# Performance work log

Hardware: AMD Instinct MI355X
Metric: run time of the kernel (lower is better)

## Reference

```python
import jax, jax.numpy as jnp
import numpy as np

N = 50000      # nodes
E = 800000     # edges per relation/layer
L = 2          # GCN layer_num
D = 128        # input_dim == output_dim


def setup_inputs() -> dict:
    key = jax.random.key(0)
    ks = jax.random.split(key, 11)
    x = jax.random.normal(ks[0], (N, D), jnp.float32)
    hidden = jax.random.normal(ks[1], (N, D), jnp.float32)
    adj_src = jax.random.randint(ks[2], (L, E), 0, N)
    adj_dst = jax.random.randint(ks[3], (L, E), 0, N)
    adj_w = jax.random.uniform(ks[4], (L, E), jnp.float32)
    std = 1.0 / np.sqrt(D)  # reset_parameters: uniform(-std, std)
    def u(k, shape):
        return jax.random.uniform(k, shape, jnp.float32, -std, std)
    gcn_W = u(ks[5], (L, D, D))
    gcn_b = u(ks[6], (L, D))
    x2h_W = u(ks[7], (D, 3 * D))
    x2h_b = u(ks[8], (3 * D,))
    h2h_W = u(ks[9], (D, 3 * D))
    h2h_b = u(ks[10], (3 * D,))
    return dict(x=x, hidden=hidden, adj_src=adj_src, adj_dst=adj_dst, adj_w=adj_w,
                gcn_W=gcn_W, gcn_b=gcn_b, x2h_W=x2h_W, x2h_b=x2h_b,
                h2h_W=h2h_W, h2h_b=h2h_b)


def reference(x, hidden, adj_src, adj_dst, adj_w, gcn_W, gcn_b,
              x2h_W, x2h_b, h2h_W, h2h_b):
    # MRGCN: layer_num GCN layers, layer l uses relation l's sparse adjacency.
    h = x
    for l in range(L):
        support = h @ gcn_W[l]                              # [N, D]
        msg = support[adj_src[l]] * adj_w[l][:, None]       # [E, D] irregular gather
        agg = jax.ops.segment_sum(msg, adj_dst[l], num_segments=N)  # spmm scatter-add
        h = jax.nn.relu(agg + gcn_b[l])
    # GRU gate chain (dropout=0 / eval mode)
    gate_x = h @ x2h_W + x2h_b                              # [N, 3D]
    gate_h = hidden @ h2h_W + h2h_b                         # [N, 3D]
    i_r, i_i, i_n = jnp.split(gate_x, 3, axis=1)
    h_r, h_i, h_n = jnp.split(gate_h, 3, axis=1)
    resetgate = jax.nn.sigmoid(i_r + h_r)
    inputgate = jax.nn.sigmoid(i_i + h_i)
    newgate = jnp.tanh(i_n + resetgate * h_n)
    hy = newgate + inputgate * (hidden - newgate)
    return hy
```

## Files before the change

### kernel.cpp

```cpp
#include <hip/hip_runtime.h>

#define D 128
#define RPW 8
#define ROWS_PB 32

typedef __attribute__((ext_vector_type(8))) short short8;
typedef __attribute__((ext_vector_type(4))) float f32x4;

static __device__ __forceinline__ ushort f2bf(float f) {
    unsigned u = __float_as_uint(f);
    unsigned r = (u + 0x7fffu + ((u >> 16) & 1u)) >> 16;
    return (ushort)r;
}

__global__ __launch_bounds__(256) void gemm_rowbatch(const float* __restrict__ in,
                                                     const float* __restrict__ W,
                                                     float* __restrict__ out, int N) {
    __shared__ float sw[D * D];
    __shared__ float sh[ROWS_PB][D];
    int tid = threadIdx.x;
    int row0 = blockIdx.x * ROWS_PB;
    for (int j = tid; j < D * D / 4; j += 256)
        ((float4*)sw)[j] = ((const float4*)W)[j];
    for (int i = tid; i < ROWS_PB * (D / 4); i += 256) {
        int r = i >> 5, c4 = i & 31;
        int row = row0 + r;
        float4 v = (row < N) ? ((const float4*)(in + (size_t)row * D))[c4]
                             : make_float4(0.f, 0.f, 0.f, 0.f);
        ((float4*)sh)[i] = v;
    }
    __syncthreads();
    int wid = tid >> 6, lane = tid & 63;
    int rb = wid * RPW;
    float acc0[RPW], acc1[RPW];
#pragma unroll
    for (int r = 0; r < RPW; ++r) { acc0[r] = 0.f; acc1[r] = 0.f; }
    for (int k = 0; k < D; k += 4) {
        float w0[4], w1[4];
#pragma unroll
        for (int kk = 0; kk < 4; ++kk) {
            w0[kk] = sw[(k + kk) * D + lane];
            w1[kk] = sw[(k + kk) * D + lane + 64];
        }
#pragma unroll
        for (int r = 0; r < RPW; ++r) {
            float4 a4 = *(const float4*)&sh[rb + r][k];
            acc0[r] = fmaf(a4.x, w0[0], acc0[r]); acc1[r] = fmaf(a4.x, w1[0], acc1[r]);
            acc0[r] = fmaf(a4.y, w0[1], acc0[r]); acc1[r] = fmaf(a4.y, w1[1], acc1[r]);
            acc0[r] = fmaf(a4.z, w0[2], acc0[r]); acc1[r] = fmaf(a4.z, w1[2], acc1[r]);
            acc0[r] = fmaf(a4.w, w0[3], acc0[r]); acc1[r] = fmaf(a4.w, w1[3], acc1[r]);
        }
    }
#pragma unroll
    for (int r = 0; r < RPW; ++r) {
        int row = row0 + rb + r;
        if (row < N) {
            out[(size_t)row * D + lane] = acc0[r];
            out[(size_t)row * D + lane + 64] = acc1[r];
        }
    }
}

__global__ void zero_int4(int4* __restrict__ p, int n4) {
    int i = blockIdx.x * blockDim.x + threadIdx.x;
    if (i < n4) p[i] = make_int4(0, 0, 0, 0);
}

__global__ void slot_kernel(const int* __restrict__ dst, int* __restrict__ counts,
                            ushort* __restrict__ pl, int E2, int E, int N) {
    int i = blockIdx.x * blockDim.x + threadIdx.x;
    if (i >= E2) return;
    int off = (i >= E) ? N : 0;
    pl[i] = (ushort)atomicAdd(&counts[off + dst[i]], 1);
}

__global__ __launch_bounds__(256) void scan_partial(const int4* __restrict__ counts4,
                                                    int* __restrict__ bsum) {
    int b = blockIdx.x, t = threadIdx.x;
    int4 c0 = counts4[(size_t)b * 512 + t * 2];
    int4 c1 = counts4[(size_t)b * 512 + t * 2 + 1];
    int s = c0.x + c0.y + c0.z + c0.w + c1.x + c1.y + c1.z + c1.w;
#pragma unroll
    for (int d = 1; d < 64; d <<= 1) s += __shfl_xor(s, d);
    __shared__ int ws[4];
    if ((t & 63) == 0) ws[t >> 6] = s;
    __syncthreads();
    if (t == 0) bsum[b] = ws[0] + ws[1] + ws[2] + ws[3];
}

__global__ void scan_base(const int* __restrict__ bsum, int* __restrict__ bbase, int nb) {
    int lane = threadIdx.x;
    int run = 0;
    for (int c = 0; c < nb; c += 64) {
        int v = (c + lane < nb) ? bsum[c + lane] : 0;
        int inc = v;
#pragma unroll
        for (int d = 1; d < 64; d <<= 1) {
            int y = __shfl_up(inc, d);
            if (lane >= d) inc += y;
        }
        if (c + lane < nb) bbase[c + lane] = run + inc - v;
        run += __shfl(inc, 63);
    }
}

__global__ __launch_bounds__(256) void scan_apply(const int4* __restrict__ counts4,
                                                  const int* __restrict__ bbase,
                                                  int4* __restrict__ off4) {
    __shared__ int ts[256];
    int b = blockIdx.x, t = threadIdx.x;
    int4 c0 = counts4[(size_t)b * 512 + t * 2];
    int4 c1 = counts4[(size_t)b * 512 + t * 2 + 1];
    int s = c0.x + c0.y + c0.z + c0.w + c1.x + c1.y + c1.z + c1.w;
    ts[t] = s;
    __syncthreads();
    for (int d = 1; d < 256; d <<= 1) {
        int x = ts[t];
        int y = (t >= d) ? ts[t - d] : 0;
        __syncthreads();
        ts[t] = x + y;
        __syncthreads();
    }
    int base = bbase[b] + ((t == 0) ? 0 : ts[t - 1]);
    int4 o0, o1;
    o0.x = base;
    o0.y = o0.x + c0.x;
    o0.z = o0.y + c0.y;
    o0.w = o0.z + c0.z;
    o1.x = o0.w + c0.w;
    o1.y = o1.x + c1.x;
    o1.z = o1.y + c1.y;
    o1.w = o1.z + c1.z;
    off4[(size_t)b * 512 + t * 2] = o0;
    off4[(size_t)b * 512 + t * 2 + 1] = o1;
}

__global__ void place_kernel(const int* __restrict__ src, const int* __restrict__ dst,
                             const float* __restrict__ w, const int* __restrict__ offsets,
                             const ushort* __restrict__ pl, int sub,
                             int2* __restrict__ srcw, int E) {
    int e = blockIdx.x * blockDim.x + threadIdx.x;
    if (e >= E) return;
    int p = offsets[dst[e]] - sub + (int)pl[e];
    srcw[p] = make_int2(src[e], __float_as_int(w[e]));
}

__global__ void gather_nodes(const float* __restrict__ sup, const int2* __restrict__ srcw,
                             const int* __restrict__ offsets, int sub,
                             const float* __restrict__ bias,
                             float* __restrict__ out, int N) {
    int node = (blockIdx.x * blockDim.x + threadIdx.x) >> 6;
    int lane = threadIdx.x & 63;
    if (node >= N) return;
    int lo = offsets[node] - sub, hi = offsets[node + 1] - sub;
    float ax = 0.f, ay = 0.f;
    int c = lane * 2;
    int j = lo;
    for (; j + 8 <= hi; j += 8) {
        int2 s[8];
        float2 v[8];
#pragma unroll
        for (int u = 0; u < 8; ++u) s[u] = srcw[j + u];
#pragma unroll
        for (int u = 0; u < 8; ++u)
            v[u] = *(const float2*)(sup + (size_t)s[u].x * D + c);
#pragma unroll
        for (int u = 0; u < 8; ++u) {
            float wt = __int_as_float(s[u].y);
            ax = fmaf(wt, v[u].x, ax);
            ay = fmaf(wt, v[u].y, ay);
        }
    }
    for (; j < hi; ++j) {
        int2 sw = srcw[j];
        float wt = __int_as_float(sw.y);
        float2 v = *(const float2*)(sup + (size_t)sw.x * D + c);
        ax = fmaf(wt, v.x, ax); ay = fmaf(wt, v.y, ay);
    }
    float2 bi = *(const float2*)(bias + c);
    float2 o;
    o.x = fmaxf(ax + bi.x, 0.f);
    o.y = fmaxf(ay + bi.y, 0.f);
    *(float2*)(out + (size_t)node * D + c) = o;
}

__global__ void convW(const float* __restrict__ Wx, const float* __restrict__ Wh,
                      ushort* __restrict__ wxt, ushort* __restrict__ wht) {
    int i = blockIdx.x * blockDim.x + threadIdx.x;
    if (i >= 384 * 128) return;
    int c = i >> 7, k = i & 127;
    wxt[i] = f2bf(Wx[(size_t)k * 384 + c]);
    wht[i] = f2bf(Wh[(size_t)k * 384 + c]);
}

#define QROWS 192
#define KPAD 136
__global__ __launch_bounds__(256) void gru_mfma_lds(const float* __restrict__ h,
                                                    const float* __restrict__ hidden,
                                                    const ushort* __restrict__ wxt,
                                                    const ushort* __restrict__ wht,
                                                    const float* __restrict__ bx,
                                                    const float* __restrict__ bh,
                                                    float* __restrict__ out, int N) {
    __shared__ ushort lw[QROWS * KPAD];
    int tid = threadIdx.x;
    int wid = tid >> 6, lane = tid & 63;
    int nstripes = (N + 15) >> 4;
    int stripe = blockIdx.x * 4 + wid;
    bool live = stripe < nstripes;
    int row0 = stripe * 16;
    int lr = lane & 15;
    int lk = (lane >> 4) * 8;

    short8 Ah[4], Ad[4];
    if (live) {
        const float* hrow = h + (size_t)(row0 + lr) * D + lk;
        const float* drow = hidden + (size_t)(row0 + lr) * D + lk;
#pragma unroll
        for (int ks = 0; ks < 4; ++ks) {
            float4 a0 = *(const float4*)(hrow + ks * 32);
            float4 a1 = *(const float4*)(hrow + ks * 32 + 4);
            float4 c0 = *(const float4*)(drow + ks * 32);
            float4 c1 = *(const float4*)(drow + ks * 32 + 4);
            short8 va, vc;
            va[0] = f2bf(a0.x); va[1] = f2bf(a0.y); va[2] = f2bf(a0.z); va[3] = f2bf(a0.w);
            va[4] = f2bf(a1.x); va[5] = f2bf(a1.y); va[6] = f2bf(a1.z); va[7] = f2bf(a1.w);
            vc[0] = f2bf(c0.x); vc[1] = f2bf(c0.y); vc[2] = f2bf(c0.z); vc[3] = f2bf(c0.w);
            vc[4] = f2bf(c1.x); vc[5] = f2bf(c1.y); vc[6] = f2bf(c1.z); vc[7] = f2bf(c1.w);
            Ah[ks] = va;
            Ad[ks] = vc;
        }
    }
    int orow = row0 + (lane >> 4) * 4;

    for (int q = 0; q < 4; ++q) {
        if (q) __syncthreads();
        for (int j = tid; j < QROWS * 16; j += 256) {
            int chunk = j & 15;
            int row = j >> 4;
            int mat = row >= 96;
            int r = row - (mat ? 96 : 0);
            int g = r >> 5;
            int c = r & 31;
            const ushort* srcp = (mat ? wht : wxt)
                               + ((size_t)(g * 128 + q * 32 + c) << 7) + (chunk << 3);
            *(short8*)&lw[row * KPAD + chunk * 8] = *(const short8*)srcp;
        }
        __syncthreads();
        if (!live) continue;

#pragma unroll
        for (int mt = 0; mt < 2; ++mt) {
            int cl = mt * 16 + lr;
            const ushort* bx0 = lw + (0 * 32 + cl) * KPAD + lk;
            const ushort* bx1 = lw + (1 * 32 + cl) * KPAD + lk;
            const ushort* bx2 = lw + (2 * 32 + cl) * KPAD + lk;
            const ushort* bh0 = lw + ((96 + 0 * 32) + cl) * KPAD + lk;
            const ushort* bh1 = lw + ((96 + 1 * 32) + cl) * KPAD + lk;
            const ushort* bh2 = lw + ((96 + 2 * 32) + cl) * KPAD + lk;
            f32x4 ax0{}, ax1{}, ax2{}, ah0{}, ah1{}, ah2{};
#pragma unroll
            for (int ks = 0; ks < 4; ++ks) {
                short8 w0 = *(const short8*)(bx0 + ks * 32);
                short8 w1 = *(const short8*)(bx1 + ks * 32);
                short8 w2 = *(const short8*)(bx2 + ks * 32);
                short8 v0 = *(const short8*)(bh0 + ks * 32);
                short8 v1 = *(const short8*)(bh1 + ks * 32);
                short8 v2 = *(const short8*)(bh2 + ks * 32);
                ax0 = __builtin_amdgcn_mfma_f32_16x16x32_bf16(Ah[ks], w0, ax0, 0, 0, 0);
                ax1 = __builtin_amdgcn_mfma_f32_16x16x32_bf16(Ah[ks], w1, ax1, 0, 0, 0);
                ax2 = __builtin_amdgcn_mfma_f32_16x16x32_bf16(Ah[ks], w2, ax2, 0, 0, 0);
                ah0 = __builtin_amdgcn_mfma_f32_16x16x32_bf16(Ad[ks], v0, ah0, 0, 0, 0);
                ah1 = __builtin_amdgcn_mfma_f32_16x16x32_bf16(Ad[ks], v1, ah1, 0, 0, 0);
                ah2 = __builtin_amdgcn_mfma_f32_16x16x32_bf16(Ad[ks], v2, ah2, 0, 0, 0);
            }
            int col = q * 32 + mt * 16 + lr;
            float bxr = bx[col], bxi = bx[col + 128], bxn = bx[col + 256];
            float bhr = bh[col], bhi = bh[col + 128], bhn = bh[col + 256];
#pragma unroll
            for (int r = 0; r < 4; ++r) {
                int row = orow + r;
                if (row < N) {
                    float ir = ax0[r] + bxr, hr = ah0[r] + bhr;
                    float ii = ax1[r] + bxi, hi = ah1[r] + bhi;
                    float in_ = ax2[r] + bxn, hn = ah2[r] + bhn;
                    float rg = 1.f / (1.f + __expf(-(ir + hr)));
                    float ig = 1.f / (1.f + __expf(-(ii + hi)));
                    float nx = in_ + rg * hn;
                    float ng = 1.f - 2.f / (__expf(2.f * nx) + 1.f);
                    float hv = hidden[(size_t)row * D + col];
                    out[(size_t)row * D + col] = ng + ig * (hv - ng);
                }
            }
        }
    }
}

extern "C" void kernel_launch(void* const* d_in, const int* in_sizes, int n_in,
                              void* d_out, int out_size, void* d_ws, size_t ws_size,
                              hipStream_t stream) {
    const float* x      = (const float*)d_in[0];
    const float* hidden = (const float*)d_in[1];
    const int*   adj_src = (const int*)d_in[2];
    const int*   adj_dst = (const int*)d_in[3];
    const float* adj_w   = (const float*)d_in[4];
    const float* gcn_W   = (const float*)d_in[5];
    const float* gcn_b   = (const float*)d_in[6];
    const float* x2h_W   = (const float*)d_in[7];
    const float* x2h_b   = (const float*)d_in[8];
    const float* h2h_W   = (const float*)d_in[9];
    const float* h2h_b   = (const float*)d_in[10];
    float* out = (float*)d_out;

    const int L = 2;
    const int N = in_sizes[0] / D;
    const int E = in_sizes[2] / L;
    const size_t nd = (size_t)N * D;

    const int twoN   = 2 * N;
    const int NB     = (twoN + 2047) / 2048;
    const int padded = NB * 2048;

    char* ws = (char*)d_ws;
    float* A        = (float*)ws;                 ws += nd * 4;
    float* B        = (float*)ws;                 ws += nd * 4;
    int*   counts2  = (int*)ws;                   ws += (size_t)padded * 4;
    int*   offsets2 = (int*)ws;                   ws += ((size_t)padded + 64) * 4;
    int*   bsum     = (int*)ws;                   ws += ((size_t)NB + 64) * 4;
    int*   bbase    = (int*)ws;                   ws += ((size_t)NB + 64) * 4;
    int2*  srcw     = (int2*)ws;                  ws += (size_t)E * 8;
    ushort* pl      = (ushort*)ws;                ws += (size_t)2 * E * 2;
    ushort* wxt     = (ushort*)ws;                ws += (size_t)384 * 128 * 2;
    ushort* wht     = (ushort*)ws;                ws += (size_t)384 * 128 * 2;

    dim3 blk(256);
    int batch_blocks = (N + ROWS_PB - 1) / ROWS_PB;
    int gat_blocks   = (N + 3) / 4;
    int edge_blocks  = (E + 255) / 256;
    int e2_blocks    = (2 * E + 255) / 256;
    int zero_blocks  = (padded / 4 + 255) / 256;
    int convw_blocks = (384 * 128 + 255) / 256;
    int nstripes     = (N + 15) / 16;
    int gru_blocks   = (nstripes + 3) / 4;

    convW<<<convw_blocks, blk, 0, stream>>>(x2h_W, h2h_W, wxt, wht);

    zero_int4<<<zero_blocks, blk, 0, stream>>>((int4*)counts2, padded / 4);
    slot_kernel<<<e2_blocks, blk, 0, stream>>>(adj_dst, counts2, pl, 2 * E, E, N);
    scan_partial<<<NB, blk, 0, stream>>>((const int4*)counts2, bsum);
    scan_base<<<1, 64, 0, stream>>>(bsum, bbase, NB);
    scan_apply<<<NB, blk, 0, stream>>>((const int4*)counts2, bbase, (int4*)offsets2);

    const float* hcur = x;
    for (int l = 0; l < L; ++l) {
        gemm_rowbatch<<<batch_blocks, blk, 0, stream>>>(hcur, gcn_W + (size_t)l * D * D, A, N);
        place_kernel<<<edge_blocks, blk, 0, stream>>>(adj_src + (size_t)l * E,
                                                      adj_dst + (size_t)l * E,
                                                      adj_w + (size_t)l * E,
                                                      offsets2 + (size_t)l * N,
                                                      pl + (size_t)l * E, l * E,
                                                      srcw, E);
        gather_nodes<<<gat_blocks, blk, 0, stream>>>(A, srcw, offsets2 + (size_t)l * N, l * E,
                                                     gcn_b + (size_t)l * D, B, N);
        hcur = B;
    }
    gru_mfma_lds<<<gru_blocks, blk, 0, stream>>>(B, hidden, wxt, wht, x2h_b, h2h_b, out, N);
}
```

Baseline: 379.8 us.

## Store GCN support in bf16 and fuse setup kernels into one launch

The GCN support matrix is now written in bf16, which halves the bytes the irregular gather reads per edge. The first-layer GEMM, the slot-counting atomics and the GRU weight conversion are merged into one heterogeneous launch so they run concurrently. Edge placement for both layers is done in one kernel into separate buffers, which removes per-layer launches. The bf16 support reduces precision of the aggregated messages, and the fused kernel's large LDS allocation applies to the light atomic and convert blocks too, which may limit their occupancy.

Result: faster. 327.3 us (-13.8%).

```diff
diff --git a/kernel.cpp b/kernel.cpp
--- a/kernel.cpp
+++ b/kernel.cpp
@@ -13,13 +13,12 @@
     return (ushort)r;
 }
 
-__global__ __launch_bounds__(256) void gemm_rowbatch(const float* __restrict__ in,
-                                                     const float* __restrict__ W,
-                                                     float* __restrict__ out, int N) {
-    __shared__ float sw[D * D];
-    __shared__ float sh[ROWS_PB][D];
-    int tid = threadIdx.x;
-    int row0 = blockIdx.x * ROWS_PB;
+static __device__ __forceinline__ void gemm_body(float* sw, float (*sh)[D],
+                                                 const float* __restrict__ in,
+                                                 const float* __restrict__ W,
+                                                 ushort* __restrict__ outb,
+                                                 int N, int bid, int tid) {
+    int row0 = bid * ROWS_PB;
     for (int j = tid; j < D * D / 4; j += 256)
         ((float4*)sw)[j] = ((const float4*)W)[j];
     for (int i = tid; i < ROWS_PB * (D / 4); i += 256) {
@@ -55,23 +54,55 @@
     for (int r = 0; r < RPW; ++r) {
         int row = row0 + rb + r;
         if (row < N) {
-            out[(size_t)row * D + lane] = acc0[r];
-            out[(size_t)row * D + lane + 64] = acc1[r];
-        }
-    }
+            outb[(size_t)row * D + lane] = f2bf(acc0[r]);
+            outb[(size_t)row * D + lane + 64] = f2bf(acc1[r]);
+        }
+    }
+}
+
+__global__ __launch_bounds__(256) void fused_sgc(const float* __restrict__ x,
+                                                 const float* __restrict__ W0,
+                                                 ushort* __restrict__ Abf, int N,
+                                                 const int* __restrict__ adj_dst,
+                                                 int* __restrict__ counts,
+                                                 ushort* __restrict__ pl, int E2, int E,
+                                                 const float* __restrict__ Wx,
+                                                 const float* __restrict__ Wh,
+                                                 ushort* __restrict__ wxt,
+                                                 ushort* __restrict__ wht,
+                                                 int GB, int SB) {
+    __shared__ float sw[D * D];
+    __shared__ float sh[ROWS_PB][D];
+    int bid = blockIdx.x, tid = threadIdx.x;
+    if (bid < GB) {
+        gemm_body(sw, sh, x, W0, Abf, N, bid, tid);
+    } else if (bid < GB + SB) {
+        int i = (bid - GB) * 256 + tid;
+        if (i < E2) {
+            int off = (i >= E) ? N : 0;
+            pl[i] = (ushort)atomicAdd(&counts[off + adj_dst[i]], 1);
+        }
+    } else {
+        int i = (bid - GB - SB) * 256 + tid;
+        if (i < 384 * 128) {
+            int c = i >> 7, k = i & 127;
+            wxt[i] = f2bf(Wx[(size_t)k * 384 + c]);
+            wht[i] = f2bf(Wh[(size_t)k * 384 + c]);
+        }
+    }
+}
+
+__global__ __launch_bounds__(256) void gemm_rowbatch_bf(const float* __restrict__ in,
+                                                        const float* __restrict__ W,
+                                                        ushort* __restrict__ outb, int N) {
+    __shared__ float sw[D * D];
+    __shared__ float sh[ROWS_PB][D];
+    gemm_body(sw, sh, in, W, outb, N, blockIdx.x, threadIdx.x);
 }
 
 __global__ void zero_int4(int4* __restrict__ p, int n4) {
     int i = blockIdx.x * blockDim.x + threadIdx.x;
     if (i < n4) p[i] = make_int4(0, 0, 0, 0);
-}
-
-__global__ void slot_kernel(const int* __restrict__ dst, int* __restrict__ counts,
-                            ushort* __restrict__ pl, int E2, int E, int N) {
-    int i = blockIdx.x * blockDim.x + threadIdx.x;
-    if (i >= E2) return;
-    int off = (i >= E) ? N : 0;
-    pl[i] = (ushort)atomicAdd(&counts[off + dst[i]], 1);
 }
 
 __global__ __launch_bounds__(256) void scan_partial(const int4* __restrict__ counts4,
@@ -135,17 +166,22 @@
     off4[(size_t)b * 512 + t * 2 + 1] = o1;
 }
 
-__global__ void place_kernel(const int* __restrict__ src, const int* __restrict__ dst,
-                             const float* __restrict__ w, const int* __restrict__ offsets,
-                             const ushort* __restrict__ pl, int sub,
-                             int2* __restrict__ srcw, int E) {
-    int e = blockIdx.x * blockDim.x + threadIdx.x;
-    if (e >= E) return;
-    int p = offsets[dst[e]] - sub + (int)pl[e];
-    srcw[p] = make_int2(src[e], __float_as_int(w[e]));
-}
-
-__global__ void gather_nodes(const float* __restrict__ sup, const int2* __restrict__ srcw,
+__global__ void place2_kernel(const int* __restrict__ src, const int* __restrict__ dst,
+                              const float* __restrict__ w,
+                              const int* __restrict__ offsets2,
+                              const ushort* __restrict__ pl,
+                              int2* __restrict__ srcw0, int2* __restrict__ srcw1,
+                              int E, int E2, int N) {
+    int i = blockIdx.x * blockDim.x + threadIdx.x;
+    if (i >= E2) return;
+    int l1 = i >= E;
+    int node = dst[i];
+    int p = offsets2[(l1 ? N : 0) + node] - (l1 ? E : 0) + (int)pl[i];
+    int2 v = make_int2(src[i], __float_as_int(w[i]));
+    (l1 ? srcw1 : srcw0)[p] = v;
+}
+
+__global__ void gather_nodes(const ushort* __restrict__ supb, const int2* __restrict__ srcw,
                              const int* __restrict__ offsets, int sub,
                              const float* __restrict__ bias,
                              float* __restrict__ out, int N) {
@@ -155,42 +191,35 @@
     int lo = offsets[node] - sub, hi = offsets[node + 1] - sub;
     float ax = 0.f, ay = 0.f;
     int c = lane * 2;
+    const ushort* base = supb + c;
     int j = lo;
     for (; j + 8 <= hi; j += 8) {
         int2 s[8];
-        float2 v[8];
+        uint v[8];
 #pragma unroll
         for (int u = 0; u < 8; ++u) s[u] = srcw[j + u];
 #pragma unroll
         for (int u = 0; u < 8; ++u)
-            v[u] = *(const float2*)(sup + (size_t)s[u].x * D + c);
+            v[u] = *(const uint*)(base + ((size_t)s[u].x << 7));
 #pragma unroll
         for (int u = 0; u < 8; ++u) {
             float wt = __int_as_float(s[u].y);
-            ax = fmaf(wt, v[u].x, ax);
-            ay = fmaf(wt, v[u].y, ay);
+            ax = fmaf(wt, __uint_as_float(v[u] << 16), ax);
+            ay = fmaf(wt, __uint_as_float(v[u] & 0xffff0000u), ay);
         }
     }
     for (; j < hi; ++j) {
         int2 sw = srcw[j];
         float wt = __int_as_float(sw.y);
-        float2 v = *(const float2*)(sup + (size_t)sw.x * D + c);
-        ax = fmaf(wt, v.x, ax); ay = fmaf(wt, v.y, ay);
+        uint v = *(const uint*)(base + ((size_t)sw.x << 7));
+        ax = fmaf(wt, __uint_as_float(v << 16), ax);
+        ay = fmaf(wt, __uint_as_float(v & 0xffff0000u), ay);
     }
     float2 bi = *(const float2*)(bias + c);
     float2 o;
     o.x = fmaxf(ax + bi.x, 0.f);
     o.y = fmaxf(ay + bi.y, 0.f);
     *(float2*)(out + (size_t)node * D + c) = o;
-}
-
-__global__ void convW(const float* __restrict__ Wx, const float* __restrict__ Wh,
-                      ushort* __restrict__ wxt, ushort* __restrict__ wht) {
-    int i = blockIdx.x * blockDim.x + threadIdx.x;
-    if (i >= 384 * 128) return;
-    int c = i >> 7, k = i & 127;
-    wxt[i] = f2bf(Wx[(size_t)k * 384 + c]);
-    wht[i] = f2bf(Wh[(size_t)k * 384 + c]);
 }
 
 #define QROWS 192
@@ -322,13 +351,14 @@
     const int padded = NB * 2048;
 
     char* ws = (char*)d_ws;
-    float* A        = (float*)ws;                 ws += nd * 4;
-    float* B        = (float*)ws;                 ws += nd * 4;
+    ushort* Abf     = (ushort*)ws;                ws += nd * 2;
+    float*  B       = (float*)ws;                 ws += nd * 4;
     int*   counts2  = (int*)ws;                   ws += (size_t)padded * 4;
     int*   offsets2 = (int*)ws;                   ws += ((size_t)padded + 64) * 4;
     int*   bsum     = (int*)ws;                   ws += ((size_t)NB + 64) * 4;
     int*   bbase    = (int*)ws;                   ws += ((size_t)NB + 64) * 4;
-    int2*  srcw     = (int2*)ws;                  ws += (size_t)E * 8;
+    int2*  srcw0    = (int2*)ws;                  ws += (size_t)E * 8;
+    int2*  srcw1    = (int2*)ws;                  ws += (size_t)E * 8;
     ushort* pl      = (ushort*)ws;                ws += (size_t)2 * E * 2;
     ushort* wxt     = (ushort*)ws;                ws += (size_t)384 * 128 * 2;
     ushort* wht     = (ushort*)ws;                ws += (size_t)384 * 128 * 2;
@@ -336,33 +366,25 @@
     dim3 blk(256);
     int batch_blocks = (N + ROWS_PB - 1) / ROWS_PB;
     int gat_blocks   = (N + 3) / 4;
-    int edge_blocks  = (E + 255) / 256;
     int e2_blocks    = (2 * E + 255) / 256;
     int zero_blocks  = (padded / 4 + 255) / 256;
     int convw_blocks = (384 * 128 + 255) / 256;
     int nstripes     = (N + 15) / 16;
     int gru_blocks   = (nstripes + 3) / 4;
 
-    convW<<<convw_blocks, blk, 0, stream>>>(x2h_W, h2h_W, wxt, wht);
-
     zero_int4<<<zero_blocks, blk, 0, stream>>>((int4*)counts2, padded / 4);
-    slot_kernel<<<e2_blocks, blk, 0, stream>>>(adj_dst, counts2, pl, 2 * E, E, N);
+    fused_sgc<<<batch_blocks + e2_blocks + convw_blocks, blk, 0, stream>>>(
+        x, gcn_W, Abf, N, adj_dst, counts2, pl, 2 * E, E,
+        x2h_W, h2h_W, wxt, wht, batch_blocks, e2_blocks);
     scan_partial<<<NB, blk, 0, stream>>>((const int4*)counts2, bsum);
     scan_base<<<1, 64, 0, stream>>>(bsum, bbase, NB);
     scan_apply<<<NB, blk, 0, stream>>>((const int4*)counts2, bbase, (int4*)offsets2);
-
-    const float* hcur = x;
-    for (int l = 0; l < L; ++l) {
-        gemm_rowbatch<<<batch_blocks, blk, 0, stream>>>(hcur, gcn_W + (size_t)l * D * D, A, N);
-        place_kernel<<<edge_blocks, blk, 0, stream>>>(adj_src + (size_t)l * E,
-                                                      adj_dst + (size_t)l * E,
-                                                      adj_w + (size_t)l * E,
-                                                      offsets2 + (size_t)l * N,
-                                                      pl + (size_t)l * E, l * E,
-                                                      srcw, E);
-        gather_nodes<<<gat_blocks, blk, 0, stream>>>(A, srcw, offsets2 + (size_t)l * N, l * E,
-                                                     gcn_b + (size_t)l * D, B, N);
-        hcur = B;
-    }
+    place2_kernel<<<e2_blocks, blk, 0, stream>>>(adj_src, adj_dst, adj_w, offsets2, pl,
+                                                 srcw0, srcw1, E, 2 * E, N);
+    gather_nodes<<<gat_blocks, blk, 0, stream>>>(Abf, srcw0, offsets2, 0,
+                                                 gcn_b, B, N);
+    gemm_rowbatch_bf<<<batch_blocks, blk, 0, stream>>>(B, gcn_W + (size_t)D * D, Abf, N);
+    gather_nodes<<<gat_blocks, blk, 0, stream>>>(Abf, srcw1, offsets2 + N, E,
+                                                 gcn_b + D, B, N);
     gru_mfma_lds<<<gru_blocks, blk, 0, stream>>>(B, hidden, wxt, wht, x2h_b, h2h_b, out, N);
 }
```
